# Kernel tuning notes

Measured on AMD Instinct MI355X. Metric: run time of the kernel, lower is better.

The kernel has to match this reference:

```python
import jax, jax.numpy as jnp
import numpy as np

LAMBDA = 0.7
RATIO = 3
EPS = 1e-6


def setup_inputs() -> dict:
    key = jax.random.key(0)
    k1, k2, k3 = jax.random.split(key, 3)
    bs, n, w, h = 8, 7, 640, 640
    preds = jax.random.normal(k1, (bs, n, w, h), dtype=jnp.float32)
    labels = jax.random.randint(k2, (bs, n, w, h), 0, 2, dtype=jnp.int32)
    training_mask = jax.random.randint(k3, (bs, w, h), 0, 2, dtype=jnp.int32)
    return {"preds": preds, "labels": labels, "training_mask": training_mask}


def _dice(S, G):
    # S, G: [C, P]; per-channel dice coefficient, then mean over channels
    num = 2.0 * jnp.sum(S * G, axis=-1)
    den = jnp.sum(S * S, axis=-1) + jnp.sum(G * G, axis=-1) + EPS
    return jnp.mean(num / den)


def _single_sample(pred, label, mask):
    # pred, label: [n, P]; mask: [P]
    P = pred.shape[-1]
    p = jax.nn.sigmoid(pred)
    pred_n = p[-1] * mask            # masked full-text prediction
    label_n = label[-1] * mask

    # --- OHEM mask M (cal_M): keep all positives + top (ratio*n_pos) hardest negatives ---
    pos = pred_n >= 0.5
    n_pos = jnp.sum(pos)
    n_neg_all = jnp.sum(~pos)
    k = n_pos * RATIO
    # sigmoid outputs are in (0,1); sentinel -1 pushes positives to the end of the descending sort
    neg_vals = jnp.where(pos, -1.0, pred_n)
    sorted_desc = -jnp.sort(-neg_vals)
    thr = sorted_desc[jnp.clip(k - 1, 0, P - 1)]  # k-th largest negative score
    ohem_active = (n_neg_all > k) & (k > 0)
    M = jnp.where(ohem_active, (pred_n >= thr).astype(jnp.float32), 1.0)

    # L_c: dice loss on OHEM-selected full-text map
    L_c = 1.0 - _dice((pred_n * M)[None, :], (label_n * M)[None, :])

    # L_s: dice loss on shrunk kernels, gated by predicted text region W
    W = (pred_n >= 0.5).astype(jnp.float32)
    L_s = 1.0 - _dice(p[:-1] * W, label[:-1] * W)

    loss = LAMBDA * L_c + (1.0 - LAMBDA) * L_s
    return L_c, L_s, loss


def reference(preds, labels, training_mask):
    bs, n, w, h = preds.shape
    preds = preds.reshape(bs, n, w * h)
    labels = labels.reshape(bs, n, w * h).astype(jnp.float32)
    mask = training_mask.reshape(bs, w * h).astype(jnp.float32)
    L_c, L_s, loss = jax.vmap(_single_sample)(preds, labels, mask)
    # reduction='mean'
    return L_c.mean(), L_s.mean(), loss.mean()
```

## Files before the change

### kernel.cpp

```cpp
#include <hip/hip_runtime.h>

#define BS   8
#define NCH  7
#define PX   409600
#define PBLK 200
#define EPSF 1e-6f

__device__ __forceinline__ float sigf(float x) {
    return 1.0f / (1.0f + __expf(-x));
}

__device__ __forceinline__ unsigned wred_u(unsigned v) {
    #pragma unroll
    for (int o = 32; o; o >>= 1) v += __shfl_down(v, o);
    return v;
}

__device__ __forceinline__ float wred_f(float v) {
    #pragma unroll
    for (int o = 32; o; o >>= 1) v += __shfl_down(v, o);
    return v;
}


__global__ __launch_bounds__(256, 4) void k_prep(const float* __restrict__ preds,
                                                 const int* __restrict__ labels,
                                                 const int* __restrict__ mask,
                                                 unsigned* __restrict__ n_pos,
                                                 unsigned* __restrict__ n_nz,
                                                 unsigned char* __restrict__ wmask,
                                                 float* __restrict__ sums) {
    int b = blockIdx.y;
    int base = (blockIdx.x * 256 + threadIdx.x) * 8;
    const float* pr = preds + ((size_t)b * NCH + 6) * PX;
    const int*   lb = labels + ((size_t)b * NCH + 6) * PX;
    const int*   mk = mask + (size_t)b * PX;

    float4 p0 = *(const float4*)(pr + base);
    float4 p1 = *(const float4*)(pr + base + 4);
    int4   l0 = *(const int4*)(lb + base);
    int4   l1 = *(const int4*)(lb + base + 4);
    int4   m0 = *(const int4*)(mk + base);
    int4   m1 = *(const int4*)(mk + base + 4);

    float ps[8] = {p0.x, p0.y, p0.z, p0.w, p1.x, p1.y, p1.z, p1.w};
    float ls[8] = {(float)l0.x, (float)l0.y, (float)l0.z, (float)l0.w,
                   (float)l1.x, (float)l1.y, (float)l1.z, (float)l1.w};
    float ms[8] = {(float)m0.x, (float)m0.y, (float)m0.z, (float)m0.w,
                   (float)m1.x, (float)m1.y, (float)m1.z, (float)m1.w};

    unsigned pos = 0, nz = 0;
    float a0 = 0.f, a1 = 0.f, a2 = 0.f;
    unsigned long long wp = 0ull;
    #pragma unroll
    for (int u = 0; u < 8; u++) {
        float pn = sigf(ps[u]) * ms[u];
        bool P = (pn >= 0.5f);
        pos += P;
        nz  += (!P && __float_as_uint(pn) != 0u);
        wp  |= ((unsigned long long)(P ? 1u : 0u)) << (8 * u);
        float ln = ls[u] * ms[u];
        a0 += pn * ln;
        a1 += pn * pn;
        a2 += ln;
    }
    *(unsigned long long*)(wmask + (size_t)b * PX + base) = wp;

    __shared__ float red[4][3];
    __shared__ unsigned ws2[2][4];
    int lane = threadIdx.x & 63, wid = threadIdx.x >> 6;
    float v0 = wred_f(a0), v1 = wred_f(a1), v2 = wred_f(a2);
    unsigned pv = wred_u(pos), zv = wred_u(nz);
    if (lane == 0) {
        red[wid][0] = v0; red[wid][1] = v1; red[wid][2] = v2;
        ws2[0][wid] = pv; ws2[1][wid] = zv;
    }
    __syncthreads();
    if (threadIdx.x < 3) {
        float tot = red[0][threadIdx.x] + red[1][threadIdx.x] +
                    red[2][threadIdx.x] + red[3][threadIdx.x];
        atomicAdd(&sums[((size_t)b * 7 + 6) * 3 + threadIdx.x], tot);
    }
    if (threadIdx.x == 64) {
        unsigned pt = ws2[0][0] + ws2[0][1] + ws2[0][2] + ws2[0][3];
        unsigned zt = ws2[1][0] + ws2[1][1] + ws2[1][2] + ws2[1][3];
        if (pt) atomicAdd(&n_pos[b], pt);
        if (zt) atomicAdd(&n_nz[b], zt);
    }
}

__global__ __launch_bounds__(256) void k_fix(const float* __restrict__ preds,
                                             const int* __restrict__ labels,
                                             const int* __restrict__ mask,
                                             const unsigned* __restrict__ n_pos,
                                             const unsigned* __restrict__ n_nz,
                                             float* __restrict__ sums) {
    int b = blockIdx.x;
    unsigned np_ = n_pos[b];
    unsigned k = np_ * 3u;
    unsigned nneg = (unsigned)PX - np_;
    bool active = (nneg > k) && (k > 0u);
    if (!active || k > n_nz[b]) return;

    const float* pr = preds + ((size_t)b * NCH + 6) * PX;
    const int*   lb = labels + ((size_t)b * NCH + 6) * PX;
    const int*   mk = mask + (size_t)b * PX;
    __shared__ unsigned hist[256];
    __shared__ unsigned sh_sel, sh_rem;
    const unsigned masks[4] = {0x00000000u, 0xFF000000u, 0xFFFF0000u, 0xFFFFFF00u};
    unsigned prefix = 0u, krem = k;
    for (int lv = 0; lv < 4; lv++) {
        int shift = 24 - 8 * lv;
        unsigned msk = masks[lv];
        for (int j = threadIdx.x; j < 256; j += 256) hist[j] = 0u;
        __syncthreads();
        for (int g = threadIdx.x; g < PX / 4; g += 256) {
            int px = g * 4;
            float4 p4 = *(const float4*)(pr + px);
            int4   m4 = *(const int4*)(mk + px);
            float pa[4] = {p4.x, p4.y, p4.z, p4.w};
            float mm[4] = {(float)m4.x, (float)m4.y, (float)m4.z, (float)m4.w};
            #pragma unroll
            for (int u = 0; u < 4; u++) {
                float pn = sigf(pa[u]) * mm[u];
                if (pn < 0.5f) {
                    unsigned bits = __float_as_uint(pn);
                    if ((bits & msk) == prefix)
                        atomicAdd(&hist[(bits >> shift) & 0xFFu], 1u);
                }
            }
        }
        __syncthreads();
        if (threadIdx.x == 0) {
            unsigned acc = 0, rem = krem, sel = 0;
            for (int i = 255; i >= 0; i--) {
                acc += hist[i];
                if (acc >= krem) { sel = (unsigned)i; rem = krem - (acc - hist[i]); break; }
            }
            sh_sel = sel; sh_rem = rem;
        }
        __syncthreads();
        prefix |= (sh_sel << shift);
        krem = sh_rem;
        __syncthreads();
    }
    float thr = __uint_as_float(prefix);

    float a0 = 0.f, a1 = 0.f, a2 = 0.f;
    for (int g = threadIdx.x; g < PX / 4; g += 256) {
        int px = g * 4;
        float4 p4 = *(const float4*)(pr + px);
        int4   l4 = *(const int4*)(lb + px);
        int4   m4 = *(const int4*)(mk + px);
        float pa[4] = {p4.x, p4.y, p4.z, p4.w};
        float la[4] = {(float)l4.x, (float)l4.y, (float)l4.z, (float)l4.w};
        float mm[4] = {(float)m4.x, (float)m4.y, (float)m4.z, (float)m4.w};
        #pragma unroll
        for (int u = 0; u < 4; u++) {
            float pn = sigf(pa[u]) * mm[u];
            float Mi = (pn >= thr) ? 1.0f : 0.0f;
            float ln = la[u] * mm[u];
            a0 += pn * ln * Mi;
            a1 += pn * pn * Mi;
            a2 += ln * Mi;
        }
    }
    __shared__ float red[4][3];
    int lane = threadIdx.x & 63, wid = threadIdx.x >> 6;
    float v0 = wred_f(a0), v1 = wred_f(a1), v2 = wred_f(a2);
    if (lane == 0) { red[wid][0] = v0; red[wid][1] = v1; red[wid][2] = v2; }
    __syncthreads();
    if (threadIdx.x < 3) {
        float tot = red[0][threadIdx.x] + red[1][threadIdx.x] +
                    red[2][threadIdx.x] + red[3][threadIdx.x];
        sums[((size_t)b * 7 + 6) * 3 + threadIdx.x] = tot;
    }
}

__global__ __launch_bounds__(256, 4) void k_sums6(const float* __restrict__ preds,
                                                  const int* __restrict__ labels,
                                                  const unsigned char* __restrict__ wmask,
                                                  float* __restrict__ sums) {
    int b = blockIdx.z, ch = blockIdx.y;
    int base = (blockIdx.x * 256 + threadIdx.x) * 8;
    const float* pr = preds + ((size_t)b * NCH + ch) * PX;
    const int*   lb = labels + ((size_t)b * NCH + ch) * PX;

    float4 p0 = *(const float4*)(pr + base);
    float4 p1 = *(const float4*)(pr + base + 4);
    int4   l0 = *(const int4*)(lb + base);
    int4   l1 = *(const int4*)(lb + base + 4);
    unsigned long long wp = *(const unsigned long long*)(wmask + (size_t)b * PX + base);

    float ps[8] = {p0.x, p0.y, p0.z, p0.w, p1.x, p1.y, p1.z, p1.w};
    float ls[8] = {(float)l0.x, (float)l0.y, (float)l0.z, (float)l0.w,
                   (float)l1.x, (float)l1.y, (float)l1.z, (float)l1.w};

    float s0 = 0.f, s1 = 0.f, s2 = 0.f;
    #pragma unroll
    for (int u = 0; u < 8; u++) {
        float W = (float)((wp >> (8 * u)) & 1ull);
        float s = sigf(ps[u]);
        float l = ls[u];
        s0 += s * l * W;
        s1 += s * s * W;
        s2 += l * W;
    }

    __shared__ float red[4][3];
    int lane = threadIdx.x & 63, wid = threadIdx.x >> 6;
    float v0 = wred_f(s0), v1 = wred_f(s1), v2 = wred_f(s2);
    if (lane == 0) { red[wid][0] = v0; red[wid][1] = v1; red[wid][2] = v2; }
    __syncthreads();
    if (threadIdx.x < 3) {
        float tot = red[0][threadIdx.x] + red[1][threadIdx.x] +
                    red[2][threadIdx.x] + red[3][threadIdx.x];
        atomicAdd(&sums[((size_t)b * 7 + ch) * 3 + threadIdx.x], tot);
    }
}

__global__ __launch_bounds__(256) void k_final(const float* __restrict__ sums,
                                               float* __restrict__ out) {
    __shared__ float fr[BS * 21];
    if (threadIdx.x < BS * 21) fr[threadIdx.x] = sums[threadIdx.x];
    __syncthreads();
    if (threadIdx.x == 0) {
        float Lc = 0.f, Ls = 0.f;
        #pragma unroll
        for (int b = 0; b < BS; b++) {
            const float* s6 = fr + (b * 7 + 6) * 3;
            Lc += 1.0f - (2.0f * s6[0]) / (s6[1] + s6[2] + EPSF);
            float acc = 0.f;
            #pragma unroll
            for (int c = 0; c < 6; c++) {
                const float* sc = fr + (b * 7 + c) * 3;
                acc += (2.0f * sc[0]) / (sc[1] + sc[2] + EPSF);
            }
            Ls += 1.0f - acc * (1.0f / 6.0f);
        }
        float lc_m = Lc * (1.0f / (float)BS);
        float ls_m = Ls * (1.0f / (float)BS);
        out[0] = lc_m;
        out[1] = ls_m;
        out[2] = 0.7f * lc_m + 0.3f * ls_m;
    }
}

extern "C" void kernel_launch(void* const* d_in, const int* in_sizes, int n_in,
                              void* d_out, int out_size, void* d_ws, size_t ws_size,
                              hipStream_t stream) {
    const float* preds = (const float*)d_in[0];
    const int* labels  = (const int*)d_in[1];
    const int* mask    = (const int*)d_in[2];
    float* out = (float*)d_out;

    unsigned* n_pos = (unsigned*)d_ws;
    unsigned* n_nz  = n_pos + BS;
    float*    sums  = (float*)(n_nz + BS);
    unsigned char* wmask = (unsigned char*)(sums + BS * 21);

    hipMemsetAsync(d_ws, 0, (2 * BS + BS * 21) * sizeof(unsigned), stream);

    hipLaunchKernelGGL(k_prep, dim3(PBLK, BS), dim3(256), 0, stream,
                       preds, labels, mask, n_pos, n_nz, wmask, sums);

    hipLaunchKernelGGL(k_fix, dim3(BS), dim3(256), 0, stream,
                       preds, labels, mask, n_pos, n_nz, sums);

    hipLaunchKernelGGL(k_sums6, dim3(PBLK, 6, BS), dim3(256), 0, stream,
                       preds, labels, wmask, sums);

    hipLaunchKernelGGL(k_final, dim3(1), dim3(256), 0, stream, sums, out);
}
```

Before: 256.4 us.

## Fuse per-channel dice sums into one pass and fold OHEM fix into final kernel

Merges the prep and six-channel sum kernels into one kernel. Each thread loads all seven channels for its pixels and computes the text-region gate W in registers instead of writing and re-reading a byte mask. The OHEM threshold-selection pass moves into the single-block final kernel, which now loops over the batch serially, and grid size is doubled with four pixels per thread. Sigmoid switches to the hardware reciprocal. This removes launches and the wmask round trip, but if the OHEM path is active for any sample, that radix-select and re-sum now run for every sample in one block instead of eight in parallel.

New measurement: 237.5 us. 1.08x faster.

```diff
diff --git a/kernel.cpp b/kernel.cpp
--- a/kernel.cpp
+++ b/kernel.cpp
@@ -3,11 +3,11 @@
 #define BS   8
 #define NCH  7
 #define PX   409600
-#define PBLK 200
+#define PBLK 400
 #define EPSF 1e-6f
 
 __device__ __forceinline__ float sigf(float x) {
-    return 1.0f / (1.0f + __expf(-x));
+    return __builtin_amdgcn_rcpf(1.0f + __expf(-x));
 }
 
 __device__ __forceinline__ unsigned wred_u(unsigned v) {
@@ -23,63 +23,87 @@
 }
 
 
-__global__ __launch_bounds__(256, 4) void k_prep(const float* __restrict__ preds,
-                                                 const int* __restrict__ labels,
-                                                 const int* __restrict__ mask,
-                                                 unsigned* __restrict__ n_pos,
-                                                 unsigned* __restrict__ n_nz,
-                                                 unsigned char* __restrict__ wmask,
-                                                 float* __restrict__ sums) {
+__global__ __launch_bounds__(256, 4) void k_fat(const float* __restrict__ preds,
+                                                const int* __restrict__ labels,
+                                                const int* __restrict__ mask,
+                                                unsigned* __restrict__ n_pos,
+                                                unsigned* __restrict__ n_nz,
+                                                float* __restrict__ sums) {
     int b = blockIdx.y;
-    int base = (blockIdx.x * 256 + threadIdx.x) * 8;
-    const float* pr = preds + ((size_t)b * NCH + 6) * PX;
-    const int*   lb = labels + ((size_t)b * NCH + 6) * PX;
+    int base = (blockIdx.x * 256 + threadIdx.x) * 4;
+    const float* pr = preds + (size_t)b * NCH * PX;
+    const int*   lb = labels + (size_t)b * NCH * PX;
     const int*   mk = mask + (size_t)b * PX;
 
-    float4 p0 = *(const float4*)(pr + base);
-    float4 p1 = *(const float4*)(pr + base + 4);
-    int4   l0 = *(const int4*)(lb + base);
-    int4   l1 = *(const int4*)(lb + base + 4);
-    int4   m0 = *(const int4*)(mk + base);
-    int4   m1 = *(const int4*)(mk + base + 4);
-
-    float ps[8] = {p0.x, p0.y, p0.z, p0.w, p1.x, p1.y, p1.z, p1.w};
-    float ls[8] = {(float)l0.x, (float)l0.y, (float)l0.z, (float)l0.w,
-                   (float)l1.x, (float)l1.y, (float)l1.z, (float)l1.w};
-    float ms[8] = {(float)m0.x, (float)m0.y, (float)m0.z, (float)m0.w,
-                   (float)m1.x, (float)m1.y, (float)m1.z, (float)m1.w};
+    int4   m4 = *(const int4*)(mk + base);
+    float4 p[7];
+    int4   l[7];
+    #pragma unroll
+    for (int c = 0; c < 7; c++) {
+        p[c] = *(const float4*)(pr + c * PX + base);
+        l[c] = *(const int4*)(lb + c * PX + base);
+    }
+
+    float ms[4] = {(float)m4.x, (float)m4.y, (float)m4.z, (float)m4.w};
+    float p6[4] = {p[6].x, p[6].y, p[6].z, p[6].w};
+    float l6[4] = {(float)l[6].x, (float)l[6].y, (float)l[6].z, (float)l[6].w};
 
     unsigned pos = 0, nz = 0;
     float a0 = 0.f, a1 = 0.f, a2 = 0.f;
-    unsigned long long wp = 0ull;
-    #pragma unroll
-    for (int u = 0; u < 8; u++) {
-        float pn = sigf(ps[u]) * ms[u];
+    float W[4];
+    #pragma unroll
+    for (int u = 0; u < 4; u++) {
+        float pn = sigf(p6[u]) * ms[u];
         bool P = (pn >= 0.5f);
         pos += P;
         nz  += (!P && __float_as_uint(pn) != 0u);
-        wp  |= ((unsigned long long)(P ? 1u : 0u)) << (8 * u);
-        float ln = ls[u] * ms[u];
+        W[u] = P ? 1.0f : 0.0f;
+        float ln = l6[u] * ms[u];
         a0 += pn * ln;
         a1 += pn * pn;
         a2 += ln;
     }
-    *(unsigned long long*)(wmask + (size_t)b * PX + base) = wp;
-
-    __shared__ float red[4][3];
+
+    float acc[18];
+    #pragma unroll
+    for (int j = 0; j < 18; j++) acc[j] = 0.f;
+    #pragma unroll
+    for (int c = 0; c < 6; c++) {
+        float ps[4] = {p[c].x, p[c].y, p[c].z, p[c].w};
+        float ls[4] = {(float)l[c].x, (float)l[c].y, (float)l[c].z, (float)l[c].w};
+        #pragma unroll
+        for (int u = 0; u < 4; u++) {
+            float s = sigf(ps[u]);
+            float lw = ls[u] * W[u];
+            acc[c]      += s * lw;
+            acc[6 + c]  += s * s * W[u];
+            acc[12 + c] += lw;
+        }
+    }
+
+    __shared__ float red[4][21];
     __shared__ unsigned ws2[2][4];
     int lane = threadIdx.x & 63, wid = threadIdx.x >> 6;
-    float v0 = wred_f(a0), v1 = wred_f(a1), v2 = wred_f(a2);
+    {
+        float v = wred_f(a0); if (lane == 0) red[wid][18] = v;
+        v = wred_f(a1);       if (lane == 0) red[wid][19] = v;
+        v = wred_f(a2);       if (lane == 0) red[wid][20] = v;
+    }
+    #pragma unroll
+    for (int j = 0; j < 18; j++) {
+        float v = wred_f(acc[j]);
+        if (lane == 0) red[wid][j] = v;
+    }
     unsigned pv = wred_u(pos), zv = wred_u(nz);
-    if (lane == 0) {
-        red[wid][0] = v0; red[wid][1] = v1; red[wid][2] = v2;
-        ws2[0][wid] = pv; ws2[1][wid] = zv;
-    }
+    if (lane == 0) { ws2[0][wid] = pv; ws2[1][wid] = zv; }
     __syncthreads();
-    if (threadIdx.x < 3) {
+    if (threadIdx.x < 21) {
         float tot = red[0][threadIdx.x] + red[1][threadIdx.x] +
                     red[2][threadIdx.x] + red[3][threadIdx.x];
-        atomicAdd(&sums[((size_t)b * 7 + 6) * 3 + threadIdx.x], tot);
+        int j = threadIdx.x;
+        int idx = (j < 18) ? (((size_t)b * 7 + (j % 6)) * 3 + (j / 6))
+                           : (((size_t)b * 7 + 6) * 3 + (j - 18));
+        atomicAdd(&sums[idx], tot);
     }
     if (threadIdx.x == 64) {
         unsigned pt = ws2[0][0] + ws2[0][1] + ws2[0][2] + ws2[0][3];
@@ -89,141 +113,101 @@
     }
 }
 
-__global__ __launch_bounds__(256) void k_fix(const float* __restrict__ preds,
-                                             const int* __restrict__ labels,
-                                             const int* __restrict__ mask,
-                                             const unsigned* __restrict__ n_pos,
-                                             const unsigned* __restrict__ n_nz,
-                                             float* __restrict__ sums) {
-    int b = blockIdx.x;
-    unsigned np_ = n_pos[b];
-    unsigned k = np_ * 3u;
-    unsigned nneg = (unsigned)PX - np_;
-    bool active = (nneg > k) && (k > 0u);
-    if (!active || k > n_nz[b]) return;
-
-    const float* pr = preds + ((size_t)b * NCH + 6) * PX;
-    const int*   lb = labels + ((size_t)b * NCH + 6) * PX;
-    const int*   mk = mask + (size_t)b * PX;
+__global__ __launch_bounds__(256) void k_final(const float* __restrict__ preds,
+                                               const int* __restrict__ labels,
+                                               const int* __restrict__ mask,
+                                               const unsigned* __restrict__ n_pos,
+                                               const unsigned* __restrict__ n_nz,
+                                               const float* __restrict__ sums,
+                                               float* __restrict__ out) {
+    __shared__ float fr[BS * 21];
+    if (threadIdx.x < BS * 21) fr[threadIdx.x] = sums[threadIdx.x];
+    __syncthreads();
+
     __shared__ unsigned hist[256];
     __shared__ unsigned sh_sel, sh_rem;
-    const unsigned masks[4] = {0x00000000u, 0xFF000000u, 0xFFFF0000u, 0xFFFFFF00u};
-    unsigned prefix = 0u, krem = k;
-    for (int lv = 0; lv < 4; lv++) {
-        int shift = 24 - 8 * lv;
-        unsigned msk = masks[lv];
-        for (int j = threadIdx.x; j < 256; j += 256) hist[j] = 0u;
-        __syncthreads();
+    __shared__ float red[4][3];
+
+    for (int b = 0; b < BS; b++) {
+        unsigned np_ = n_pos[b];
+        unsigned k = np_ * 3u;
+        unsigned nneg = (unsigned)PX - np_;
+        bool active = (nneg > k) && (k > 0u);
+        if (!active || k > n_nz[b]) continue;
+
+        const float* pr = preds + ((size_t)b * NCH + 6) * PX;
+        const int*   lb = labels + ((size_t)b * NCH + 6) * PX;
+        const int*   mk = mask + (size_t)b * PX;
+        unsigned prefix = 0u, krem = k;
+        const unsigned masks[4] = {0x00000000u, 0xFF000000u, 0xFFFF0000u, 0xFFFFFF00u};
+        for (int lv = 0; lv < 4; lv++) {
+            int shift = 24 - 8 * lv;
+            unsigned msk = masks[lv];
+            hist[threadIdx.x] = 0u;
+            __syncthreads();
+            for (int g = threadIdx.x; g < PX / 4; g += 256) {
+                int px = g * 4;
+                float4 p4 = *(const float4*)(pr + px);
+                int4   m4 = *(const int4*)(mk + px);
+                float pa[4] = {p4.x, p4.y, p4.z, p4.w};
+                float mm[4] = {(float)m4.x, (float)m4.y, (float)m4.z, (float)m4.w};
+                #pragma unroll
+                for (int u = 0; u < 4; u++) {
+                    float pn = sigf(pa[u]) * mm[u];
+                    if (pn < 0.5f) {
+                        unsigned bits = __float_as_uint(pn);
+                        if ((bits & msk) == prefix)
+                            atomicAdd(&hist[(bits >> shift) & 0xFFu], 1u);
+                    }
+                }
+            }
+            __syncthreads();
+            if (threadIdx.x == 0) {
+                unsigned acc = 0, rem = krem, sel = 0;
+                for (int i = 255; i >= 0; i--) {
+                    acc += hist[i];
+                    if (acc >= krem) { sel = (unsigned)i; rem = krem - (acc - hist[i]); break; }
+                }
+                sh_sel = sel; sh_rem = rem;
+            }
+            __syncthreads();
+            prefix |= (sh_sel << shift);
+            krem = sh_rem;
+            __syncthreads();
+        }
+        float thr = __uint_as_float(prefix);
+
+        float a0 = 0.f, a1 = 0.f, a2 = 0.f;
         for (int g = threadIdx.x; g < PX / 4; g += 256) {
             int px = g * 4;
             float4 p4 = *(const float4*)(pr + px);
+            int4   l4 = *(const int4*)(lb + px);
             int4   m4 = *(const int4*)(mk + px);
             float pa[4] = {p4.x, p4.y, p4.z, p4.w};
+            float la[4] = {(float)l4.x, (float)l4.y, (float)l4.z, (float)l4.w};
             float mm[4] = {(float)m4.x, (float)m4.y, (float)m4.z, (float)m4.w};
             #pragma unroll
             for (int u = 0; u < 4; u++) {
                 float pn = sigf(pa[u]) * mm[u];
-                if (pn < 0.5f) {
-                    unsigned bits = __float_as_uint(pn);
-                    if ((bits & msk) == prefix)
-                        atomicAdd(&hist[(bits >> shift) & 0xFFu], 1u);
-                }
-            }
-        }
+                float Mi = (pn >= thr) ? 1.0f : 0.0f;
+                float ln = la[u] * mm[u];
+                a0 += pn * ln * Mi;
+                a1 += pn * pn * Mi;
+                a2 += ln * Mi;
+            }
+        }
+        int lane = threadIdx.x & 63, wid = threadIdx.x >> 6;
+        float v0 = wred_f(a0), v1 = wred_f(a1), v2 = wred_f(a2);
+        if (lane == 0) { red[wid][0] = v0; red[wid][1] = v1; red[wid][2] = v2; }
         __syncthreads();
-        if (threadIdx.x == 0) {
-            unsigned acc = 0, rem = krem, sel = 0;
-            for (int i = 255; i >= 0; i--) {
-                acc += hist[i];
-                if (acc >= krem) { sel = (unsigned)i; rem = krem - (acc - hist[i]); break; }
-            }
-            sh_sel = sel; sh_rem = rem;
+        if (threadIdx.x < 3) {
+            fr[(b * 7 + 6) * 3 + threadIdx.x] =
+                red[0][threadIdx.x] + red[1][threadIdx.x] +
+                red[2][threadIdx.x] + red[3][threadIdx.x];
         }
         __syncthreads();
-        prefix |= (sh_sel << shift);
-        krem = sh_rem;
-        __syncthreads();
-    }
-    float thr = __uint_as_float(prefix);
-
-    float a0 = 0.f, a1 = 0.f, a2 = 0.f;
-    for (int g = threadIdx.x; g < PX / 4; g += 256) {
-        int px = g * 4;
-        float4 p4 = *(const float4*)(pr + px);
-        int4   l4 = *(const int4*)(lb + px);
-        int4   m4 = *(const int4*)(mk + px);
-        float pa[4] = {p4.x, p4.y, p4.z, p4.w};
-        float la[4] = {(float)l4.x, (float)l4.y, (float)l4.z, (float)l4.w};
-        float mm[4] = {(float)m4.x, (float)m4.y, (float)m4.z, (float)m4.w};
-        #pragma unroll
-        for (int u = 0; u < 4; u++) {
-            float pn = sigf(pa[u]) * mm[u];
-            float Mi = (pn >= thr) ? 1.0f : 0.0f;
-            float ln = la[u] * mm[u];
-            a0 += pn * ln * Mi;
-            a1 += pn * pn * Mi;
-            a2 += ln * Mi;
-        }
-    }
-    __shared__ float red[4][3];
-    int lane = threadIdx.x & 63, wid = threadIdx.x >> 6;
-    float v0 = wred_f(a0), v1 = wred_f(a1), v2 = wred_f(a2);
-    if (lane == 0) { red[wid][0] = v0; red[wid][1] = v1; red[wid][2] = v2; }
-    __syncthreads();
-    if (threadIdx.x < 3) {
-        float tot = red[0][threadIdx.x] + red[1][threadIdx.x] +
-                    red[2][threadIdx.x] + red[3][threadIdx.x];
-        sums[((size_t)b * 7 + 6) * 3 + threadIdx.x] = tot;
-    }
-}
-
-__global__ __launch_bounds__(256, 4) void k_sums6(const float* __restrict__ preds,
-                                                  const int* __restrict__ labels,
-                                                  const unsigned char* __restrict__ wmask,
-                                                  float* __restrict__ sums) {
-    int b = blockIdx.z, ch = blockIdx.y;
-    int base = (blockIdx.x * 256 + threadIdx.x) * 8;
-    const float* pr = preds + ((size_t)b * NCH + ch) * PX;
-    const int*   lb = labels + ((size_t)b * NCH + ch) * PX;
-
-    float4 p0 = *(const float4*)(pr + base);
-    float4 p1 = *(const float4*)(pr + base + 4);
-    int4   l0 = *(const int4*)(lb + base);
-    int4   l1 = *(const int4*)(lb + base + 4);
-    unsigned long long wp = *(const unsigned long long*)(wmask + (size_t)b * PX + base);
-
-    float ps[8] = {p0.x, p0.y, p0.z, p0.w, p1.x, p1.y, p1.z, p1.w};
-    float ls[8] = {(float)l0.x, (float)l0.y, (float)l0.z, (float)l0.w,
-                   (float)l1.x, (float)l1.y, (float)l1.z, (float)l1.w};
-
-    float s0 = 0.f, s1 = 0.f, s2 = 0.f;
-    #pragma unroll
-    for (int u = 0; u < 8; u++) {
-        float W = (float)((wp >> (8 * u)) & 1ull);
-        float s = sigf(ps[u]);
-        float l = ls[u];
-        s0 += s * l * W;
-        s1 += s * s * W;
-        s2 += l * W;
-    }
-
-    __shared__ float red[4][3];
-    int lane = threadIdx.x & 63, wid = threadIdx.x >> 6;
-    float v0 = wred_f(s0), v1 = wred_f(s1), v2 = wred_f(s2);
-    if (lane == 0) { red[wid][0] = v0; red[wid][1] = v1; red[wid][2] = v2; }
-    __syncthreads();
-    if (threadIdx.x < 3) {
-        float tot = red[0][threadIdx.x] + red[1][threadIdx.x] +
-                    red[2][threadIdx.x] + red[3][threadIdx.x];
-        atomicAdd(&sums[((size_t)b * 7 + ch) * 3 + threadIdx.x], tot);
-    }
-}
-
-__global__ __launch_bounds__(256) void k_final(const float* __restrict__ sums,
-                                               float* __restrict__ out) {
-    __shared__ float fr[BS * 21];
-    if (threadIdx.x < BS * 21) fr[threadIdx.x] = sums[threadIdx.x];
-    __syncthreads();
+    }
+
     if (threadIdx.x == 0) {
         float Lc = 0.f, Ls = 0.f;
         #pragma unroll
@@ -257,18 +241,12 @@
     unsigned* n_pos = (unsigned*)d_ws;
     unsigned* n_nz  = n_pos + BS;
     float*    sums  = (float*)(n_nz + BS);
-    unsigned char* wmask = (unsigned char*)(sums + BS * 21);
 
     hipMemsetAsync(d_ws, 0, (2 * BS + BS * 21) * sizeof(unsigned), stream);
 
-    hipLaunchKernelGGL(k_prep, dim3(PBLK, BS), dim3(256), 0, stream,
-                       preds, labels, mask, n_pos, n_nz, wmask, sums);
-
-    hipLaunchKernelGGL(k_fix, dim3(BS), dim3(256), 0, stream,
+    hipLaunchKernelGGL(k_fat, dim3(PBLK, BS), dim3(256), 0, stream,
                        preds, labels, mask, n_pos, n_nz, sums);
 
-    hipLaunchKernelGGL(k_sums6, dim3(PBLK, 6, BS), dim3(256), 0, stream,
-                       preds, labels, wmask, sums);
-
-    hipLaunchKernelGGL(k_final, dim3(1), dim3(256), 0, stream, sums, out);
-}
+    hipLaunchKernelGGL(k_final, dim3(1), dim3(256), 0, stream,
+                       preds, labels, mask, n_pos, n_nz, sums, out);
+}
```
